# Kernel tuning notes

Measured on AMD Instinct MI355X. Metric: run time of the kernel, lower is better.

## Reference

```python
import math
import jax, jax.numpy as jnp
import numpy as np

SEQ_LEN = 2048
PATCH = 16
D_MODEL = 512
N_HEADS = 8
D_FF = 2048
E_LAYERS = 3
KERNELS = (8, 4, 2, 1)


def _pos_embedding(L, d):
    # standard sinusoidal PE, matches PositionalEmbedding
    pos = np.arange(L, dtype=np.float32)[:, None]
    div = np.exp(np.arange(0, d, 2, dtype=np.float32) * (-math.log(10000.0) / d))
    pe = np.zeros((L, d), dtype=np.float32)
    pe[:, 0::2] = np.sin(pos * div)
    pe[:, 1::2] = np.cos(pos * div)
    return jnp.asarray(pe)


def _layer_norm(x, g, b, eps=1e-5):
    mu = jnp.mean(x, axis=-1, keepdims=True)
    var = jnp.mean(jnp.square(x - mu), axis=-1, keepdims=True)
    return (x - mu) * jax.lax.rsqrt(var + eps) * g + b


def setup_inputs() -> dict:
    key = jax.random.key(0)
    ks = jax.random.split(key, 12)
    bs, c = 8, 32
    s = 0.02
    L, D = E_LAYERS, D_MODEL
    inp = {
        "x_enc": jax.random.normal(ks[0], (bs, SEQ_LEN, c), jnp.float32),
        "W_emb": jax.random.normal(ks[1], (PATCH, D), jnp.float32) * s,
        "Wq": jax.random.normal(ks[2], (L, D, D), jnp.float32) * s,
        "bq": jnp.zeros((L, D), jnp.float32),
        "Wk": jax.random.normal(ks[3], (L, D, D), jnp.float32) * s,
        "bk": jnp.zeros((L, D), jnp.float32),
        "Wv": jax.random.normal(ks[4], (L, D, D), jnp.float32) * s,
        "bv": jnp.zeros((L, D), jnp.float32),
        "Wo": jax.random.normal(ks[5], (L, D, D), jnp.float32) * s,
        "bo": jnp.zeros((L, D), jnp.float32),
        "ln1_g": jnp.ones((L, D), jnp.float32),
        "ln1_b": jnp.zeros((L, D), jnp.float32),
        "W1": jax.random.normal(ks[6], (L, D, D_FF), jnp.float32) * s,
        "b1": jnp.zeros((L, D_FF), jnp.float32),
        "W2": jax.random.normal(ks[7], (L, D_FF, D), jnp.float32) * s,
        "b2": jnp.zeros((L, D), jnp.float32),
        "ln2_g": jnp.ones((L, D), jnp.float32),
        "ln2_b": jnp.zeros((L, D), jnp.float32),
        "lnf_g": jnp.ones((D,), jnp.float32),
        "lnf_b": jnp.zeros((D,), jnp.float32),
    }
    return inp


def reference(x_enc, W_emb, Wq, bq, Wk, bk, Wv, bv, Wo, bo,
              ln1_g, ln1_b, W1, b1, W2, b2, ln2_g, ln2_b, lnf_g, lnf_b):
    bs, t, c = x_enc.shape
    B = bs * c
    # channel-independent sequences: (bs, t, c) -> (bs*c, t)
    x = jnp.transpose(x_enc, (0, 2, 1)).reshape(B, t)

    # multi-scale interval sampling + patch embedding per scale
    p_lens = [(t // k) // PATCH for k in KERNELS]  # [16, 32, 64, 128]
    toks = []
    for k in KERNELS:
        xs = x[:, ::k]  # interval sampling (replicate-pad unfold [...,0] == stride-k sampling here)
        patches = xs.reshape(B, -1, PATCH)  # non-overlapping patches (stride == patch_len)
        toks.append(patches @ W_emb)  # value embedding, no bias
    h = jnp.concatenate(toks, axis=1)  # (B, L_tot=240, D)

    # multi-scale positional embedding: downsample pe of finest scale
    pe = _pos_embedding(p_lens[-1], D_MODEL)
    pos = jnp.concatenate([pe[::k] for k in KERNELS], axis=0)  # (240, D)
    h = h + pos[None]

    # block-diagonal scale-independence mask
    seg = np.concatenate([np.full(pl, i, dtype=np.int32) for i, pl in enumerate(p_lens)])
    allowed = jnp.asarray(seg[:, None] == seg[None, :])  # (240, 240) True = attend

    hd = D_MODEL // N_HEADS
    scale = 1.0 / math.sqrt(hd)
    Ltot = h.shape[1]
    for i in range(E_LAYERS):
        q = (h @ Wq[i] + bq[i]).reshape(B, Ltot, N_HEADS, hd)
        k_ = (h @ Wk[i] + bk[i]).reshape(B, Ltot, N_HEADS, hd)
        v_ = (h @ Wv[i] + bv[i]).reshape(B, Ltot, N_HEADS, hd)
        scores = jnp.einsum('blhd,bmhd->bhlm', q, k_) * scale
        scores = jnp.where(allowed[None, None], scores, -jnp.inf)
        attn = jax.nn.softmax(scores, axis=-1)
        o = jnp.einsum('bhlm,bmhd->blhd', attn, v_).reshape(B, Ltot, D_MODEL)
        o = o @ Wo[i] + bo[i]
        h = _layer_norm(h + o, ln1_g[i], ln1_b[i])
        f = jax.nn.gelu(h @ W1[i] + b1[i]) @ W2[i] + b2[i]
        h = _layer_norm(h + f, ln2_g[i], ln2_b[i])
    return _layer_norm(h, lnf_g, lnf_b)
```

## Files before the change

kernel.cpp:

```cpp
#include <hip/hip_runtime.h>
#include <hip/hip_bf16.h>

typedef short bf16x8 __attribute__((ext_vector_type(8)));
typedef float f32x4 __attribute__((ext_vector_type(4)));
using bf16 = __hip_bfloat16;

#define GLOBAL_LOAD_LDS16(g, l)                                                          \
    __builtin_amdgcn_global_load_lds((const __attribute__((address_space(1))) unsigned int*)(g), \
                                     (__attribute__((address_space(3))) unsigned int*)(l), \
                                     16, 0, 0)

static __device__ __forceinline__ float gelu_f(float x) {
    float u = 1.5957691216057308f * x * (1.0f + 0.044715f * x * x);
    return x / (1.0f + __expf(-u));
}

static __device__ __forceinline__ unsigned pack_bf16(float lo, float hi) {
    union { bf16 h; unsigned short u; } a, b;
    a.h = __float2bfloat16(lo);
    b.h = __float2bfloat16(hi);
    return ((unsigned)b.u << 16) | (unsigned)a.u;
}

__global__ __launch_bounds__(256) void transpose_f32_bf16(const float* __restrict__ in,
                                                          bf16* __restrict__ out,
                                                          int R, int C, size_t zso) {
    __shared__ float tile[32][33];
    size_t zi = (size_t)blockIdx.z * R * C;
    size_t zo = (size_t)blockIdx.z * zso;
    int c0 = blockIdx.x * 32, r0 = blockIdx.y * 32;
    int tx = threadIdx.x & 31, ty = threadIdx.x >> 5;
    #pragma unroll
    for (int i = 0; i < 32; i += 8) {
        int r = r0 + ty + i, c = c0 + tx;
        if (r < R && c < C) tile[ty + i][tx] = in[zi + (size_t)r * C + c];
    }
    __syncthreads();
    #pragma unroll
    for (int i = 0; i < 32; i += 8) {
        int c = c0 + ty + i, r = r0 + tx;
        if (c < C && r < R) out[zo + (size_t)c * R + r] = __float2bfloat16(tile[tx][ty + i]);
    }
}

__global__ __launch_bounds__(256) void concat_bias(const float* __restrict__ bq,
                                                   const float* __restrict__ bk,
                                                   const float* __restrict__ bv,
                                                   float* __restrict__ out) {
    int i = blockIdx.x * 256 + threadIdx.x;
    if (i < 3 * 1536) {
        int L = i / 1536, r = i - L * 1536;
        float v = (r < 512) ? bq[L * 512 + r]
                : (r < 1024) ? bk[L * 512 + r - 512]
                             : bv[L * 512 + r - 1024];
        out[i] = v;
    }
}

__global__ __launch_bounds__(256) void transpose_v(const bf16* __restrict__ in,
                                                   bf16* __restrict__ out) {
    __shared__ bf16 tile[32][33];
    int b = blockIdx.z;
    int d0 = blockIdx.x * 32, t0 = blockIdx.y * 32;
    int tx = threadIdx.x & 31, ty = threadIdx.x >> 5;
    #pragma unroll
    for (int i = 0; i < 32; i += 8) {
        int tt = t0 + ty + i, dd = d0 + tx;
        if (tt < 240) tile[ty + i][tx] = in[((size_t)b * 240 + tt) * 1536 + 1024 + dd];
    }
    __syncthreads();
    #pragma unroll
    for (int i = 0; i < 32; i += 8) {
        int dd = d0 + ty + i, tt = t0 + tx;
        if (tt < 240) out[((size_t)b * 512 + dd) * 240 + tt] = tile[tx][ty + i];
    }
}

__global__ __launch_bounds__(256) void embed_kernel(const float* __restrict__ x_enc,
                                                    const float* __restrict__ W_emb,
                                                    bf16* __restrict__ h) {
    int row = blockIdx.x;
    int b = row / 240, l = row - b * 240;
    int s = (l < 16) ? 0 : (l < 48) ? 1 : (l < 112) ? 2 : 3;
    int len = 16 << s;
    int off = len - 16;
    int kk = 8 >> s;
    int j = l - off;
    int bs_i = b >> 5, c_i = b & 31;
    __shared__ float xv[16];
    int t = threadIdx.x;
    if (t < 16) {
        int tau = (j * 16 + t) * kk;
        xv[t] = x_enc[((size_t)bs_i * 2048 + tau) * 32 + c_i];
    }
    __syncthreads();
    int pe_row = j * kk;
    const float NEG2LN = -0.035977892078032f;
    for (int d = t; d < 512; d += 256) {
        float acc = 0.f;
        #pragma unroll
        for (int i = 0; i < 16; ++i) acc += xv[i] * W_emb[i * 512 + d];
        int di = d >> 1;
        float ang = (float)pe_row * expf((float)di * NEG2LN);
        float pos = (d & 1) ? cosf(ang) : sinf(ang);
        h[(size_t)row * 512 + d] = __float2bfloat16(acc + pos);
    }
}

__global__ __launch_bounds__(256) void gemm_bt(const bf16* __restrict__ A,
                                               const bf16* __restrict__ Bt,
                                               const float* __restrict__ bias,
                                               bf16* __restrict__ C,
                                               int M, int N, int K, int act) {
    __shared__ __align__(16) bf16 smem[2 * 128 * 64];
    bf16* As = smem;
    bf16* Bs = smem + 128 * 64;
    const int t = threadIdx.x;
    const int wave = t >> 6, lane = t & 63;
    const int quad = lane >> 4, l16 = lane & 15;
    const int m0 = blockIdx.y * 128, n0 = blockIdx.x * 128;
    const int wm = (wave >> 1) * 64, wn = (wave & 1) * 64;

    f32x4 acc[4][4];
    #pragma unroll
    for (int a = 0; a < 4; ++a)
        #pragma unroll
        for (int b = 0; b < 4; ++b)
            #pragma unroll
            for (int r = 0; r < 4; ++r) acc[a][b][r] = 0.0f;

    const int srow = lane >> 3;
    const int schunk = (lane & 7) ^ srow;
    const bf16* Abase = A + (size_t)(m0 + wave * 32 + srow) * K + schunk * 8;
    const bf16* Bbase = Bt + (size_t)(n0 + wave * 32 + srow) * K + schunk * 8;

    for (int k0 = 0; k0 < K; k0 += 64) {
        __syncthreads();
        #pragma unroll
        for (int p = 0; p < 4; ++p) {
            GLOBAL_LOAD_LDS16(Abase + (size_t)p * 8 * K + k0, As + (wave * 4 + p) * 512);
            GLOBAL_LOAD_LDS16(Bbase + (size_t)p * 8 * K + k0, Bs + (wave * 4 + p) * 512);
        }
        __syncthreads();
        #pragma unroll
        for (int kt = 0; kt < 2; ++kt) {
            bf16x8 af[4], bfr[4];
            #pragma unroll
            for (int mi = 0; mi < 4; ++mi) {
                int row = wm + mi * 16 + l16;
                af[mi] = *(const bf16x8*)(&As[row * 64 + (((kt << 2) + quad) ^ (l16 & 7)) * 8]);
            }
            #pragma unroll
            for (int ni = 0; ni < 4; ++ni) {
                int row = wn + ni * 16 + l16;
                bfr[ni] = *(const bf16x8*)(&Bs[row * 64 + (((kt << 2) + quad) ^ (l16 & 7)) * 8]);
            }
            #pragma unroll
            for (int mi = 0; mi < 4; ++mi)
                #pragma unroll
                for (int ni = 0; ni < 4; ++ni)
                    acc[mi][ni] = __builtin_amdgcn_mfma_f32_16x16x32_bf16(af[mi], bfr[ni],
                                                                         acc[mi][ni], 0, 0, 0);
        }
    }

    const int oddl = l16 & 1;
    #pragma unroll
    for (int ni = 0; ni < 4; ++ni) {
        int col = n0 + wn + ni * 16 + l16;
        float bv = bias[col];
        #pragma unroll
        for (int mi = 0; mi < 4; ++mi) {
            float v0 = acc[mi][ni][0] + bv;
            float v1 = acc[mi][ni][1] + bv;
            float v2 = acc[mi][ni][2] + bv;
            float v3 = acc[mi][ni][3] + bv;
            if (act) {
                v0 = gelu_f(v0); v1 = gelu_f(v1);
                v2 = gelu_f(v2); v3 = gelu_f(v3);
            }
            float p0 = __shfl_xor(v0, 1);
            float p1 = __shfl_xor(v1, 1);
            float p2 = __shfl_xor(v2, 1);
            float p3 = __shfl_xor(v3, 1);
            float lo0 = oddl ? p1 : v0, hi0 = oddl ? v1 : p0;
            float lo1 = oddl ? p3 : v2, hi1 = oddl ? v3 : p2;
            int r0 = oddl ? 1 : 0;
            size_t rowb = (size_t)(m0 + wm + mi * 16 + quad * 4);
            unsigned* c0p = (unsigned*)(C + (rowb + r0) * N + (col & ~1));
            unsigned* c1p = (unsigned*)(C + (rowb + r0 + 2) * N + (col & ~1));
            *c0p = pack_bf16(lo0, hi0);
            *c1p = pack_bf16(lo1, hi1);
        }
    }
}

template<int LEN>
__global__ __launch_bounds__(256) void attn_mfma(const bf16* __restrict__ qkv,
                                                 const bf16* __restrict__ vt,
                                                 bf16* __restrict__ o) {
    constexpr int NT = LEN / 16;
    constexpr int KT = (LEN >= 32) ? (LEN / 32) : 1;
    constexpr int PST = (LEN == 16) ? 40 : (LEN + 8);
    constexpr int SLABS = LEN / 16;
    constexpr int OFF = LEN - 16;
    __shared__ __align__(16) bf16 Plds[4 * 16 * PST];

    const int t = threadIdx.x;
    const int wave = t >> 6, lane = t & 63;
    const int quad = lane >> 4, l16 = lane & 15;
    const int task = blockIdx.x * 4 + wave;
    const int b = task / (8 * SLABS);
    const int rem = task - b * (8 * SLABS);
    const int h = rem / SLABS;
    const int slab = rem - h * SLABS;

    const size_t qbase = ((size_t)b * 240 + OFF) * 1536 + h * 64;
    const size_t obase = ((size_t)b * 240 + OFF) * 512 + h * 64;

    const bf16* qp = qkv + qbase + (size_t)(slab * 16 + l16) * 1536 + quad * 8;
    bf16x8 qf0 = *(const bf16x8*)qp;
    bf16x8 qf1 = *(const bf16x8*)(qp + 32);

    f32x4 sacc[NT];
    #pragma unroll
    for (int nt = 0; nt < NT; ++nt) {
        const bf16* kp = qkv + qbase + 512 + (size_t)(nt * 16 + l16) * 1536 + quad * 8;
        bf16x8 kf0 = *(const bf16x8*)kp;
        bf16x8 kf1 = *(const bf16x8*)(kp + 32);
        f32x4 a = {0.f, 0.f, 0.f, 0.f};
        a = __builtin_amdgcn_mfma_f32_16x16x32_bf16(qf0, kf0, a, 0, 0, 0);
        a = __builtin_amdgcn_mfma_f32_16x16x32_bf16(qf1, kf1, a, 0, 0, 0);
        sacc[nt] = a;
    }

    float mx[4], sm[4];
    #pragma unroll
    for (int r = 0; r < 4; ++r) mx[r] = -3.0e38f;
    #pragma unroll
    for (int nt = 0; nt < NT; ++nt)
        #pragma unroll
        for (int r = 0; r < 4; ++r) {
            sacc[nt][r] *= 0.125f;
            mx[r] = fmaxf(mx[r], sacc[nt][r]);
        }
    #pragma unroll
    for (int msk = 1; msk < 16; msk <<= 1)
        #pragma unroll
        for (int r = 0; r < 4; ++r) mx[r] = fmaxf(mx[r], __shfl_xor(mx[r], msk));
    #pragma unroll
    for (int r = 0; r < 4; ++r) sm[r] = 0.f;
    #pragma unroll
    for (int nt = 0; nt < NT; ++nt)
        #pragma unroll
        for (int r = 0; r < 4; ++r) {
            float p = __expf(sacc[nt][r] - mx[r]);
            sacc[nt][r] = p;
            sm[r] += p;
        }
    #pragma unroll
    for (int msk = 1; msk < 16; msk <<= 1)
        #pragma unroll
        for (int r = 0; r < 4; ++r) sm[r] += __shfl_xor(sm[r], msk);
    float inv[4];
    #pragma unroll
    for (int r = 0; r < 4; ++r) inv[r] = 1.f / sm[r];

    bf16* pw = Plds + wave * 16 * PST;
    #pragma unroll
    for (int nt = 0; nt < NT; ++nt)
        #pragma unroll
        for (int r = 0; r < 4; ++r)
            pw[(quad * 4 + r) * PST + nt * 16 + l16] =
                __float2bfloat16(sacc[nt][r] * inv[r]);
    if (LEN == 16) {
        #pragma unroll
        for (int r = 0; r < 4; ++r)
            pw[(quad * 4 + r) * PST + 16 + l16] = __float2bfloat16(0.f);
    }
    __syncthreads();

    f32x4 oacc[4];
    #pragma unroll
    for (int n4 = 0; n4 < 4; ++n4) {
        f32x4 z = {0.f, 0.f, 0.f, 0.f};
        oacc[n4] = z;
    }
    #pragma unroll
    for (int kt = 0; kt < KT; ++kt) {
        bf16x8 pf = *(const bf16x8*)&pw[l16 * PST + kt * 32 + quad * 8];
        #pragma unroll
        for (int n4 = 0; n4 < 4; ++n4) {
            const bf16* vp = vt + ((size_t)b * 512 + h * 64 + n4 * 16 + l16) * 240
                              + OFF + kt * 32 + quad * 8;
            bf16x8 vf = *(const bf16x8*)vp;
            oacc[n4] = __builtin_amdgcn_mfma_f32_16x16x32_bf16(pf, vf, oacc[n4], 0, 0, 0);
        }
    }
    #pragma unroll
    for (int n4 = 0; n4 < 4; ++n4)
        #pragma unroll
        for (int r = 0; r < 4; ++r)
            o[obase + (size_t)(slab * 16 + quad * 4 + r) * 512 + n4 * 16 + l16] =
                __float2bfloat16(oacc[n4][r]);
}

__global__ __launch_bounds__(256) void ln_kernel(const bf16* x, const bf16* res,
                                                 const float* __restrict__ g,
                                                 const float* __restrict__ bta,
                                                 bf16* out_bf, float* out_f) {
    int row = blockIdx.x;
    int t = threadIdx.x;
    const bf16* xr = x + (size_t)row * 512;
    float v0 = __bfloat162float(xr[t]);
    float v1 = __bfloat162float(xr[t + 256]);
    if (res) {
        const bf16* rr = res + (size_t)row * 512;
        v0 += __bfloat162float(rr[t]);
        v1 += __bfloat162float(rr[t + 256]);
    }
    float s = v0 + v1, ss = v0 * v0 + v1 * v1;
    #pragma unroll
    for (int mk = 1; mk < 64; mk <<= 1) { s += __shfl_xor(s, mk); ss += __shfl_xor(ss, mk); }
    __shared__ float red[8];
    int wave = t >> 6, lane = t & 63;
    if (lane == 0) { red[wave * 2] = s; red[wave * 2 + 1] = ss; }
    __syncthreads();
    s = red[0] + red[2] + red[4] + red[6];
    ss = red[1] + red[3] + red[5] + red[7];
    float mu = s * (1.f / 512.f);
    float var = ss * (1.f / 512.f) - mu * mu;
    float inv = rsqrtf(var + 1e-5f);
    float y0 = (v0 - mu) * inv * g[t] + bta[t];
    float y1 = (v1 - mu) * inv * g[t + 256] + bta[t + 256];
    if (out_bf) {
        bf16* orow = out_bf + (size_t)row * 512;
        orow[t] = __float2bfloat16(y0);
        orow[t + 256] = __float2bfloat16(y1);
    } else {
        float* orow = out_f + (size_t)row * 512;
        orow[t] = y0;
        orow[t + 256] = y1;
    }
}

extern "C" void kernel_launch(void* const* d_in, const int* in_sizes, int n_in,
                              void* d_out, int out_size, void* d_ws, size_t ws_size,
                              hipStream_t stream) {
    const float* x_enc = (const float*)d_in[0];
    const float* W_emb = (const float*)d_in[1];
    const float* Wq    = (const float*)d_in[2];
    const float* bq    = (const float*)d_in[3];
    const float* Wk    = (const float*)d_in[4];
    const float* bk    = (const float*)d_in[5];
    const float* Wv    = (const float*)d_in[6];
    const float* bv    = (const float*)d_in[7];
    const float* Wo    = (const float*)d_in[8];
    const float* bo    = (const float*)d_in[9];
    const float* ln1_g = (const float*)d_in[10];
    const float* ln1_b = (const float*)d_in[11];
    const float* W1    = (const float*)d_in[12];
    const float* b1    = (const float*)d_in[13];
    const float* W2    = (const float*)d_in[14];
    const float* b2    = (const float*)d_in[15];
    const float* ln2_g = (const float*)d_in[16];
    const float* ln2_b = (const float*)d_in[17];
    const float* lnf_g = (const float*)d_in[18];
    const float* lnf_b = (const float*)d_in[19];

    const int ROWS = 256 * 240;
    char* ws = (char*)d_ws;
    const size_t Hb = (size_t)ROWS * 512 * 2;
    bf16* h    = (bf16*)(ws);
    bf16* qkv  = (bf16*)(ws + Hb);
    bf16* oa   = (bf16*)(ws + 4 * Hb);
    bf16* scr2 = (bf16*)(ws + 5 * Hb);
    bf16* mid  = qkv;
    bf16* WqkvT = (bf16*)(ws + 6 * Hb);
    bf16* WoT  = WqkvT + (size_t)3 * 1536 * 512;
    bf16* W1T  = WoT + (size_t)3 * 512 * 512;
    bf16* W2T  = W1T + (size_t)3 * 512 * 2048;
    float* bcat = (float*)(W2T + (size_t)3 * 2048 * 512);

    bf16* vt     = scr2;
    bf16* oproj  = scr2;
    bf16* ffnout = scr2;

    dim3 blk(256);
    transpose_f32_bf16<<<dim3(16, 16, 3), blk, 0, stream>>>(Wq, WqkvT, 512, 512, (size_t)1536 * 512);
    transpose_f32_bf16<<<dim3(16, 16, 3), blk, 0, stream>>>(Wk, WqkvT + (size_t)512 * 512, 512, 512, (size_t)1536 * 512);
    transpose_f32_bf16<<<dim3(16, 16, 3), blk, 0, stream>>>(Wv, WqkvT + (size_t)1024 * 512, 512, 512, (size_t)1536 * 512);
    transpose_f32_bf16<<<dim3(16, 16, 3), blk, 0, stream>>>(Wo, WoT, 512, 512, (size_t)512 * 512);
    transpose_f32_bf16<<<dim3(64, 16, 3), blk, 0, stream>>>(W1, W1T, 512, 2048, (size_t)512 * 2048);
    transpose_f32_bf16<<<dim3(16, 64, 3), blk, 0, stream>>>(W2, W2T, 2048, 512, (size_t)2048 * 512);
    concat_bias<<<18, blk, 0, stream>>>(bq, bk, bv, bcat);

    embed_kernel<<<ROWS, blk, 0, stream>>>(x_enc, W_emb, h);

    for (int L = 0; L < 3; ++L) {
        size_t wo = (size_t)L * 512 * 512;
        size_t w1o = (size_t)L * 512 * 2048;
        gemm_bt<<<dim3(12, 480), blk, 0, stream>>>(h, WqkvT + (size_t)L * 1536 * 512,
                                                   bcat + L * 1536, qkv, ROWS, 1536, 512, 0);
        transpose_v<<<dim3(16, 8, 256), blk, 0, stream>>>(qkv, vt);
        attn_mfma<16><<<512, blk, 0, stream>>>(qkv, vt, oa);
        attn_mfma<32><<<1024, blk, 0, stream>>>(qkv, vt, oa);
        attn_mfma<64><<<2048, blk, 0, stream>>>(qkv, vt, oa);
        attn_mfma<128><<<4096, blk, 0, stream>>>(qkv, vt, oa);
        gemm_bt<<<dim3(4, 480), blk, 0, stream>>>(oa, WoT + wo, bo + L * 512, oproj, ROWS, 512, 512, 0);
        ln_kernel<<<ROWS, blk, 0, stream>>>(h, oproj, ln1_g + L * 512, ln1_b + L * 512, h, nullptr);
        gemm_bt<<<dim3(16, 480), blk, 0, stream>>>(h, W1T + w1o, b1 + L * 2048, mid, ROWS, 2048, 512, 1);
        gemm_bt<<<dim3(4, 480), blk, 0, stream>>>(mid, W2T + w1o, b2 + L * 512, ffnout, ROWS, 512, 2048, 0);
        ln_kernel<<<ROWS, blk, 0, stream>>>(h, ffnout, ln2_g + L * 512, ln2_b + L * 512, h, nullptr);
    }
    ln_kernel<<<ROWS, blk, 0, stream>>>(h, nullptr, lnf_g, lnf_b, nullptr, (float*)d_out);
}
```

Baseline: 2.967 ms.

## Replace LDS-staged GEMM with direct global-to-register MFMA GEMM using wider tiles

The shared-memory staged GEMM, with its two block barriers per K step, is replaced by a templated kernel in which each wave loads its MFMA operand fragments straight from global memory into registers. The block tile grows to 128x256, with each wave computing 64x128, and the K loop is fully unrolled in chunks of 512. The aim is to remove LDS traffic and block synchronisation. In exchange, operands shared between waves are no longer reused through LDS, so the kernel relies on L1/L2 to absorb repeated loads, uses strided uncoalesced 16-byte global reads, and needs a much larger accumulator register footprint that may lower occupancy.

```diff
diff --git a/kernel.cpp b/kernel.cpp
--- a/kernel.cpp
+++ b/kernel.cpp
@@ -4,11 +4,6 @@
 typedef short bf16x8 __attribute__((ext_vector_type(8)));
 typedef float f32x4 __attribute__((ext_vector_type(4)));
 using bf16 = __hip_bfloat16;
-
-#define GLOBAL_LOAD_LDS16(g, l)                                                          \
-    __builtin_amdgcn_global_load_lds((const __attribute__((address_space(1))) unsigned int*)(g), \
-                                     (__attribute__((address_space(3))) unsigned int*)(l), \
-                                     16, 0, 0)
 
 static __device__ __forceinline__ float gelu_f(float x) {
     float u = 1.5957691216057308f * x * (1.0f + 0.044715f * x * x);
@@ -107,58 +102,43 @@
     }
 }
 
-__global__ __launch_bounds__(256) void gemm_bt(const bf16* __restrict__ A,
-                                               const bf16* __restrict__ Bt,
-                                               const float* __restrict__ bias,
-                                               bf16* __restrict__ C,
-                                               int M, int N, int K, int act) {
-    __shared__ __align__(16) bf16 smem[2 * 128 * 64];
-    bf16* As = smem;
-    bf16* Bs = smem + 128 * 64;
+template<int K>
+__global__ __launch_bounds__(256) void gemm_direct(const bf16* __restrict__ A,
+                                                   const bf16* __restrict__ Bt,
+                                                   const float* __restrict__ bias,
+                                                   bf16* __restrict__ C,
+                                                   int N, int act) {
     const int t = threadIdx.x;
     const int wave = t >> 6, lane = t & 63;
     const int quad = lane >> 4, l16 = lane & 15;
-    const int m0 = blockIdx.y * 128, n0 = blockIdx.x * 128;
-    const int wm = (wave >> 1) * 64, wn = (wave & 1) * 64;
-
-    f32x4 acc[4][4];
-    #pragma unroll
-    for (int a = 0; a < 4; ++a)
-        #pragma unroll
-        for (int b = 0; b < 4; ++b)
+    const int m0 = blockIdx.y * 128 + (wave >> 1) * 64;
+    const int n0 = blockIdx.x * 256 + (wave & 1) * 128;
+
+    f32x4 acc[4][8];
+    #pragma unroll
+    for (int mi = 0; mi < 4; ++mi)
+        #pragma unroll
+        for (int ni = 0; ni < 8; ++ni)
             #pragma unroll
-            for (int r = 0; r < 4; ++r) acc[a][b][r] = 0.0f;
-
-    const int srow = lane >> 3;
-    const int schunk = (lane & 7) ^ srow;
-    const bf16* Abase = A + (size_t)(m0 + wave * 32 + srow) * K + schunk * 8;
-    const bf16* Bbase = Bt + (size_t)(n0 + wave * 32 + srow) * K + schunk * 8;
-
-    for (int k0 = 0; k0 < K; k0 += 64) {
-        __syncthreads();
-        #pragma unroll
-        for (int p = 0; p < 4; ++p) {
-            GLOBAL_LOAD_LDS16(Abase + (size_t)p * 8 * K + k0, As + (wave * 4 + p) * 512);
-            GLOBAL_LOAD_LDS16(Bbase + (size_t)p * 8 * K + k0, Bs + (wave * 4 + p) * 512);
-        }
-        __syncthreads();
-        #pragma unroll
-        for (int kt = 0; kt < 2; ++kt) {
-            bf16x8 af[4], bfr[4];
+            for (int r = 0; r < 4; ++r) acc[mi][ni][r] = 0.0f;
+
+    const bf16* Ab = A + (size_t)(m0 + l16) * K + quad * 8;
+    const bf16* Bb = Bt + (size_t)(n0 + l16) * K + quad * 8;
+
+    for (int ko = 0; ko < K; ko += 512) {
+        #pragma unroll
+        for (int kc = 0; kc < 512; kc += 32) {
+            bf16x8 af[4], bfr[8];
             #pragma unroll
-            for (int mi = 0; mi < 4; ++mi) {
-                int row = wm + mi * 16 + l16;
-                af[mi] = *(const bf16x8*)(&As[row * 64 + (((kt << 2) + quad) ^ (l16 & 7)) * 8]);
-            }
+            for (int mi = 0; mi < 4; ++mi)
+                af[mi] = *(const bf16x8*)(Ab + (size_t)mi * 16 * K + ko + kc);
             #pragma unroll
-            for (int ni = 0; ni < 4; ++ni) {
-                int row = wn + ni * 16 + l16;
-                bfr[ni] = *(const bf16x8*)(&Bs[row * 64 + (((kt << 2) + quad) ^ (l16 & 7)) * 8]);
-            }
+            for (int ni = 0; ni < 8; ++ni)
+                bfr[ni] = *(const bf16x8*)(Bb + (size_t)ni * 16 * K + ko + kc);
             #pragma unroll
             for (int mi = 0; mi < 4; ++mi)
                 #pragma unroll
-                for (int ni = 0; ni < 4; ++ni)
+                for (int ni = 0; ni < 8; ++ni)
                     acc[mi][ni] = __builtin_amdgcn_mfma_f32_16x16x32_bf16(af[mi], bfr[ni],
                                                                          acc[mi][ni], 0, 0, 0);
         }
@@ -166,8 +146,8 @@
 
     const int oddl = l16 & 1;
     #pragma unroll
-    for (int ni = 0; ni < 4; ++ni) {
-        int col = n0 + wn + ni * 16 + l16;
+    for (int ni = 0; ni < 8; ++ni) {
+        int col = n0 + ni * 16 + l16;
         float bv = bias[col];
         #pragma unroll
         for (int mi = 0; mi < 4; ++mi) {
@@ -186,7 +166,7 @@
             float lo0 = oddl ? p1 : v0, hi0 = oddl ? v1 : p0;
             float lo1 = oddl ? p3 : v2, hi1 = oddl ? v3 : p2;
             int r0 = oddl ? 1 : 0;
-            size_t rowb = (size_t)(m0 + wm + mi * 16 + quad * 4);
+            size_t rowb = (size_t)(m0 + mi * 16 + quad * 4);
             unsigned* c0p = (unsigned*)(C + (rowb + r0) * N + (col & ~1));
             unsigned* c1p = (unsigned*)(C + (rowb + r0 + 2) * N + (col & ~1));
             *c0p = pack_bf16(lo0, hi0);
@@ -400,17 +380,17 @@
     for (int L = 0; L < 3; ++L) {
         size_t wo = (size_t)L * 512 * 512;
         size_t w1o = (size_t)L * 512 * 2048;
-        gemm_bt<<<dim3(12, 480), blk, 0, stream>>>(h, WqkvT + (size_t)L * 1536 * 512,
-                                                   bcat + L * 1536, qkv, ROWS, 1536, 512, 0);
+        gemm_direct<512><<<dim3(6, 480), blk, 0, stream>>>(h, WqkvT + (size_t)L * 1536 * 512,
+                                                           bcat + L * 1536, qkv, 1536, 0);
         transpose_v<<<dim3(16, 8, 256), blk, 0, stream>>>(qkv, vt);
         attn_mfma<16><<<512, blk, 0, stream>>>(qkv, vt, oa);
         attn_mfma<32><<<1024, blk, 0, stream>>>(qkv, vt, oa);
         attn_mfma<64><<<2048, blk, 0, stream>>>(qkv, vt, oa);
         attn_mfma<128><<<4096, blk, 0, stream>>>(qkv, vt, oa);
-        gemm_bt<<<dim3(4, 480), blk, 0, stream>>>(oa, WoT + wo, bo + L * 512, oproj, ROWS, 512, 512, 0);
+        gemm_direct<512><<<dim3(2, 480), blk, 0, stream>>>(oa, WoT + wo, bo + L * 512, oproj, 512, 0);
         ln_kernel<<<ROWS, blk, 0, stream>>>(h, oproj, ln1_g + L * 512, ln1_b + L * 512, h, nullptr);
-        gemm_bt<<<dim3(16, 480), blk, 0, stream>>>(h, W1T + w1o, b1 + L * 2048, mid, ROWS, 2048, 512, 1);
-        gemm_bt<<<dim3(4, 480), blk, 0, stream>>>(mid, W2T + w1o, b2 + L * 512, ffnout, ROWS, 512, 2048, 0);
+        gemm_direct<512><<<dim3(8, 480), blk, 0, stream>>>(h, W1T + w1o, b1 + L * 2048, mid, 2048, 1);
+        gemm_direct<2048><<<dim3(2, 480), blk, 0, stream>>>(mid, W2T + w1o, b2 + L * 512, ffnout, 512, 0);
         ln_kernel<<<ROWS, blk, 0, stream>>>(h, ffnout, ln2_g + L * 512, ln2_b + L * 512, h, nullptr);
     }
     ln_kernel<<<ROWS, blk, 0, stream>>>(h, nullptr, lnf_g, lnf_b, nullptr, (float*)d_out);
```

Result: slower. 5.476 ms (+84.6%).
